# Performance work log

Hardware: AMD Instinct MI355X
Metric: run time of the kernel (lower is better)

## Reference

```python
import jax, jax.numpy as jnp
import numpy as np

MODEL_DIM = 2048
HEAD_DIM = 64
STATE_DIM = 128
EXPAND = 2
CHUNK = 64
INNER = EXPAND * MODEL_DIM          # 4096
NHEADS = INNER // HEAD_DIM          # 64
IN_PROJ = INNER + 2 * STATE_DIM + NHEADS  # 4416
B_SZ = 2
SEQ = 4096


def segsum(x):
    """Stable segment sum: x (..., T) -> (..., T, T) with -inf above diagonal."""
    T = x.shape[-1]
    mask_strict = jnp.tril(jnp.ones((T, T), dtype=bool), -1)
    # element [d, e] = x[d] on strictly-lower triangle, 0 elsewhere
    xt = jnp.where(mask_strict, x[..., :, None], 0.0)
    seg = jnp.cumsum(xt, axis=-2)
    mask = jnp.tril(jnp.ones((T, T), dtype=bool), 0)
    return jnp.where(mask, seg, -jnp.inf)


def ssd(x, A, B, C, chunk):
    """Mamba-2 SSD. x:(b,L,h,p), A:(b,L,h), B/C:(b,L,n) shared over heads."""
    b, L, h, p = x.shape
    n = B.shape[-1]
    c = L // chunk
    x = x.reshape(b, c, chunk, h, p)
    A = A.reshape(b, c, chunk, h).transpose(0, 3, 1, 2)  # (b,h,c,l)
    B = B.reshape(b, c, chunk, n)
    C = C.reshape(b, c, chunk, n)

    A_cs = jnp.cumsum(A, axis=-1)                        # (b,h,c,l)
    Lm = jnp.exp(segsum(A))                              # (b,h,c,l,l)
    # 1. diagonal (intra-chunk) output
    Y_diag = jnp.einsum('bcln,bcsn,bhcls,bcshp->bclhp', C, B, Lm, x)
    # 2. per-chunk states
    decay_states = jnp.exp(A_cs[..., -1:] - A_cs)        # (b,h,c,l)
    states = jnp.einsum('bcln,bhcl,bclhp->bchpn', B, decay_states, x)
    states = jnp.concatenate([jnp.zeros_like(states[:, :1]), states], axis=1)
    # 3. inter-chunk recurrence
    A_chunk = jnp.pad(A_cs[..., -1], ((0, 0), (0, 0), (1, 0)))   # (b,h,c+1)
    decay_chunk = jnp.exp(segsum(A_chunk))               # (b,h,c+1,c+1)
    new_states = jnp.einsum('bhzc,bchpn->bzhpn', decay_chunk, states)
    states_prev, final_state = new_states[:, :-1], new_states[:, -1]
    # 4. state -> output
    Y_off = jnp.einsum('bcln,bchpn,bhcl->bclhp', C, states_prev, jnp.exp(A_cs))
    Y = (Y_diag + Y_off).reshape(b, L, h, p)
    return Y, final_state


def setup_inputs() -> dict:
    key = jax.random.key(0)
    ks = jax.random.split(key, 6)
    u = jax.random.normal(ks[0], (B_SZ, SEQ, MODEL_DIM), jnp.float32)
    W_in = jax.random.normal(ks[1], (IN_PROJ, MODEL_DIM), jnp.float32) * 0.02
    b_in = jnp.zeros((IN_PROJ,), jnp.float32)
    W_out = jax.random.normal(ks[2], (MODEL_DIM, INNER), jnp.float32) * 0.02
    b_out = jnp.zeros((MODEL_DIM,), jnp.float32)
    # A_log = log(uniform(1, 16)) per Mamba-2 init
    A_log = jnp.log(jax.random.uniform(ks[3], (NHEADS,), jnp.float32, 1.0, 16.0))
    # dt_bias = inv-softplus of dt ~ loguniform(1e-3, 1e-1)
    dt = jnp.exp(jax.random.uniform(ks[4], (NHEADS,), jnp.float32)
                 * (np.log(0.1) - np.log(0.001)) + np.log(0.001))
    dt = jnp.clip(dt, 1e-4, None)
    dt_bias = dt + jnp.log(-jnp.expm1(-dt))
    return {'u': u, 'W_in': W_in, 'b_in': b_in, 'W_out': W_out,
            'b_out': b_out, 'A_log': A_log, 'dt_bias': dt_bias}


def reference(u, W_in, b_in, W_out, b_out, A_log, dt_bias):
    xBCdt = u @ W_in.T + b_in                       # (b, L, IN_PROJ)
    x, Bm, Cm, dt = jnp.split(
        xBCdt, [INNER, INNER + STATE_DIM, INNER + 2 * STATE_DIM], axis=-1)
    A = -jnp.exp(A_log)                             # (h,)
    dt = jax.nn.softplus(dt + dt_bias)              # (b, L, h)
    x = x.reshape(B_SZ, SEQ, NHEADS, HEAD_DIM)
    y, final_state = ssd(x * dt[..., None], A * dt, Bm, Cm, CHUNK)
    y = y.reshape(B_SZ, SEQ, INNER)
    y = y @ W_out.T + b_out
    return y, final_state
```

## Files before the change

### kernel.cpp

```cpp
#include <hip/hip_runtime.h>
#include <hip/hip_bf16.h>

typedef __hip_bfloat16 bf16;
typedef __attribute__((ext_vector_type(8))) short short8;
typedef __attribute__((ext_vector_type(4))) float f32x4;

#define MODEL_DIM 2048
#define INNER     4096
#define NHEADS    64
#define HEAD_DIM  64
#define STATE_DIM 128
#define IN_PROJ   4416
#define NPAD      4608
#define BSZ       2
#define SEQ       4096
#define CHUNKL    64
#define NTOK      (BSZ*SEQ)
#define NCHUNK    (SEQ/CHUNKL)

#define WAITV0() asm volatile("s_waitcnt vmcnt(0)" ::: "memory")
#define BAR()    __builtin_amdgcn_s_barrier()
#define SCHEDB() __builtin_amdgcn_sched_barrier(0)
#define WAITLG(N) do { asm volatile("s_waitcnt lgkmcnt(" #N ")" ::: "memory"); SCHEDB(); } while (0)

#define SWZ(x) ((x) ^ ((((x) >> 7) & 7) << 4))

static __device__ __forceinline__ void gload_lds16(const bf16* g, bf16* l) {
  __builtin_amdgcn_global_load_lds((const __attribute__((address_space(1))) void*)g,
                                   (__attribute__((address_space(3))) void*)l, 16, 0, 0);
}

static __device__ __forceinline__ unsigned lds_u32(const void* p) {
  return (unsigned)(unsigned long long)(const __attribute__((address_space(3))) char*)p;
}

static __device__ __forceinline__ short8 ds_read128(unsigned addr) {
  short8 r;
  asm volatile("ds_read_b128 %0, %1" : "=v"(r) : "v"(addr));
  return r;
}

static __device__ __forceinline__ void stage_unit(const bf16* __restrict__ P, int K,
                                                  int blockRow, int kt,
                                                  char* region, int unit, int t) {
  int o = unit * 8192 + (t << 4);
  int lb = SWZ(o);
  int row = lb >> 7, colb = lb & 127;
  gload_lds16(P + (size_t)(blockRow + row) * K + kt + (colb >> 1), (bf16*)(region + o));
}

#define MFMA_BLK(MLO, MHI, NLO, NHI)                                                    \
  __builtin_amdgcn_s_setprio(1);                                                       \
  _Pragma("unroll") for (int mf = (MLO); mf < (MHI); ++mf)                             \
    _Pragma("unroll") for (int nf = (NLO); nf < (NHI); ++nf)                           \
      _Pragma("unroll") for (int ks = 0; ks < 2; ++ks)                                 \
        acc[mf][nf] = __builtin_amdgcn_mfma_f32_16x16x32_bf16(a[mf][ks], b[nf][ks],    \
                                                              acc[mf][nf], 0, 0, 0);  \
  __builtin_amdgcn_s_setprio(0);

template<int BN>
static __device__ __forceinline__ void gemm_core1(
    const bf16* __restrict__ Ag, const bf16* __restrict__ Bg,
    int K, int NT, int bm, int bn, char* lds, f32x4 (&acc)[8][BN / 64]) {
  constexpr int NR = BN / 64;
  constexpr int BB = 32768 + NR * 8192;
  const int t = threadIdx.x;
  const int lane = t & 63;
  const int wid = t >> 6, wm = wid >> 2, wn = wid & 3;
  const unsigned x16 = (unsigned)(lane & 7) << 4;
  const unsigned kb0 = (unsigned)(lane >> 4) << 4;
  const unsigned ldsB = lds_u32(lds);
  const unsigned aRow0 = (unsigned)(wm * 128 + (lane & 15)) * 128;
  const unsigned bRow0 = (unsigned)(wn * (BN / 4) + (lane & 15)) * 128;

#pragma unroll
  for (int u = 0; u < 4; ++u) stage_unit(Ag, K, bm, 0, lds, u, t);
#pragma unroll
  for (int u = 0; u < NR; ++u) stage_unit(Bg, K, bn, 0, lds + 32768, u, t);
  WAITV0();
  BAR();

  int cur = 0;
  for (int tt = 0; tt < NT; ++tt) {
    char* oth = lds + (cur ^ 1) * BB;
    const unsigned aB = ldsB + (unsigned)(cur * BB);
    const unsigned bB = aB + 32768;
    const bool st = (tt + 1 < NT);

    if (st) {
      const int kt1 = (tt + 1) * 64;
#pragma unroll
      for (int u = 0; u < 4; ++u) stage_unit(Ag, K, bm, kt1, oth, u, t);
#pragma unroll
      for (int u = 0; u < NR; ++u) stage_unit(Bg, K, bn, kt1, oth + 32768, u, t);
    }

    short8 a[8][2], b[NR][2];
#pragma unroll
    for (int mf = 0; mf < 4; ++mf)
#pragma unroll
      for (int ks = 0; ks < 2; ++ks)
        a[mf][ks] = ds_read128(aB + aRow0 + mf * 2048 + (((unsigned)(ks * 64) + kb0) ^ x16));
#pragma unroll
    for (int nf = 0; nf < 2; ++nf)
#pragma unroll
      for (int ks = 0; ks < 2; ++ks)
        b[nf][ks] = ds_read128(bB + bRow0 + nf * 2048 + (((unsigned)(ks * 64) + kb0) ^ x16));
#pragma unroll
    for (int mf = 4; mf < 8; ++mf)
#pragma unroll
      for (int ks = 0; ks < 2; ++ks)
        a[mf][ks] = ds_read128(aB + aRow0 + mf * 2048 + (((unsigned)(ks * 64) + kb0) ^ x16));
#pragma unroll
    for (int nf = 2; nf < NR; ++nf)
#pragma unroll
      for (int ks = 0; ks < 2; ++ks)
        b[nf][ks] = ds_read128(bB + bRow0 + nf * 2048 + (((unsigned)(ks * 64) + kb0) ^ x16));

    if constexpr (NR == 4) WAITLG(12); else WAITLG(10);
    MFMA_BLK(0, 4, 0, 2);
    if constexpr (NR == 4) WAITLG(4);  else WAITLG(2);
    MFMA_BLK(4, 8, 0, 2);
    WAITLG(0);
    MFMA_BLK(0, 8, 2, NR);

    if (st) WAITV0();
    BAR();
    cur ^= 1;
  }
}

__global__ __launch_bounds__(512, 2)
void gemm_in256(const bf16* __restrict__ A, const bf16* __restrict__ Bw,
                const float* __restrict__ bias, bf16* __restrict__ x_bf,
                bf16* __restrict__ B_bf, bf16* __restrict__ C_bf, float* __restrict__ dtraw) {
  __shared__ char lds[2 * (32768 + 3 * 8192)];
  int nwg = gridDim.x, bid = blockIdx.x;
  int cpx = nwg >> 3;
  int sb = (bid & 7) * cpx + (bid >> 3);
  int bx = sb % (NPAD / 192), by = sb / (NPAD / 192);
  int bm = by * 256, bn = bx * 192;
  f32x4 acc[8][3] = {};
  gemm_core1<192>(A, Bw, MODEL_DIM, MODEL_DIM / 64, bm, bn, lds, acc);
  const int lane = threadIdx.x & 63, wid = threadIdx.x >> 6;
  const int wm = wid >> 2, wn = wid & 3;
#pragma unroll
  for (int mf = 0; mf < 8; ++mf)
#pragma unroll
    for (int nf = 0; nf < 3; ++nf)
#pragma unroll
      for (int r = 0; r < 4; ++r) {
        int row = bm + wm * 128 + mf * 16 + (lane >> 4) * 4 + r;
        int col = bn + wn * 48 + nf * 16 + (lane & 15);
        float v = acc[mf][nf][r] + ((col < IN_PROJ) ? bias[col] : 0.f);
        if (col < 4096)       x_bf[(size_t)row * 4096 + col]         = __float2bfloat16(v);
        else if (col < 4224)  B_bf[(size_t)row * 128 + (col - 4096)] = __float2bfloat16(v);
        else if (col < 4352)  C_bf[(size_t)row * 128 + (col - 4224)] = __float2bfloat16(v);
        else if (col < 4416)  dtraw[(size_t)row * 64 + (col - 4352)] = v;
      }
}

__global__ __launch_bounds__(512, 2)
void gemm_out256(const bf16* __restrict__ A, const bf16* __restrict__ Bw,
                 const float* __restrict__ bias, float* __restrict__ C) {
  __shared__ char lds[2 * (32768 + 4 * 8192)];
  int nwg = gridDim.x, bid = blockIdx.x;
  int cpx = nwg >> 3;
  int sb = (bid & 7) * cpx + (bid >> 3);
  int bx = sb % (MODEL_DIM / 256), by = sb / (MODEL_DIM / 256);
  int bm = by * 256, bn = bx * 256;
  f32x4 acc[8][4] = {};
  gemm_core1<256>(A, Bw, INNER, INNER / 64, bm, bn, lds, acc);
  const int lane = threadIdx.x & 63, wid = threadIdx.x >> 6;
  const int wm = wid >> 2, wn = wid & 3;
#pragma unroll
  for (int mf = 0; mf < 8; ++mf)
#pragma unroll
    for (int nf = 0; nf < 4; ++nf)
#pragma unroll
      for (int r = 0; r < 4; ++r) {
        int row = bm + wm * 128 + mf * 16 + (lane >> 4) * 4 + r;
        int col = bn + wn * 64 + nf * 16 + (lane & 15);
        C[(size_t)row * MODEL_DIM + col] = acc[mf][nf][r] + bias[col];
      }
}

__global__ __launch_bounds__(256) void conv_f32_to_bf16(const float* __restrict__ src,
                                                        bf16* __restrict__ dst, int n4) {
  int i = blockIdx.x * 256 + threadIdx.x;
  if (i >= n4) return;
  float4 v = *(const float4*)(src + (size_t)i * 4);
  bf16* d = dst + (size_t)i * 4;
  d[0] = __float2bfloat16(v.x); d[1] = __float2bfloat16(v.y);
  d[2] = __float2bfloat16(v.z); d[3] = __float2bfloat16(v.w);
}

__global__ __launch_bounds__(256) void conv_win_pad(const float* __restrict__ W,
                                                    bf16* __restrict__ dst) {
  int i = blockIdx.x * 256 + threadIdx.x;
  int row = (i * 4) >> 11;
  int col = (i * 4) & 2047;
  bf16* d = dst + (size_t)i * 4;
  if (row < IN_PROJ) {
    float4 v = *(const float4*)(W + (size_t)row * 2048 + col);
    d[0] = __float2bfloat16(v.x); d[1] = __float2bfloat16(v.y);
    d[2] = __float2bfloat16(v.z); d[3] = __float2bfloat16(v.w);
  } else {
    bf16 z = __float2bfloat16(0.f);
    d[0] = z; d[1] = z; d[2] = z; d[3] = z;
  }
}

__global__ __launch_bounds__(256)
void prep_small(const float* __restrict__ dtraw, const float* __restrict__ A_log,
                const float* __restrict__ dt_bias, float* __restrict__ dts,
                float* __restrict__ a_dt) {
  int i = blockIdx.x * 256 + threadIdx.x;
  int h = i & 63;
  float z = dtraw[i] + dt_bias[h];
  float dt = (z > 20.f) ? z : log1pf(expf(z));
  dts[i] = dt;
  a_dt[i] = -expf(A_log[h]) * dt;
}

#define LP 72
__global__ __launch_bounds__(256)
void ssd_fused_kernel(const bf16* __restrict__ x_bf, const bf16* __restrict__ B_bf,
                      const float* __restrict__ dts_g, const float* __restrict__ a_dt,
                      float* __restrict__ acs_g, bf16* __restrict__ states_g,
                      float* __restrict__ out_fs) {
  __shared__ bf16 xT[2][32 * LP];
  __shared__ bf16 BT[2][128 * LP];
  __shared__ float sc_s[64];
  __shared__ float dfac_s[1];
  int blk = blockIdx.x;
  int pg = blk & 1, h = (blk >> 1) & 63, b = blk >> 7;
  int t = threadIdx.x, lane = t & 63, w = t >> 6;
  int lx = t >> 2, sx = t & 3;
  int lB = t >> 2, sB = t & 3;

  f32x4 S4[4] = {};
  short8 rx, rB[4]; float ra = 0.f, rdt = 0.f;
  {
    int tb = b * SEQ;
    rx = *(const short8*)(x_bf + (size_t)(tb + lx) * 4096 + h * 64 + pg * 32 + sx * 8);
#pragma unroll
    for (int k = 0; k < 4; ++k)
      rB[k] = *(const short8*)(B_bf + (size_t)(tb + lB) * 128 + sB * 32 + k * 8);
    if (t < 64) { ra = a_dt[(size_t)(tb + t) * 64 + h]; rdt = dts_g[(size_t)(tb + t) * 64 + h]; }
  }

  for (int c = 0; c < 64; ++c) {
    int cn = (c < 63) ? c + 1 : 63;
    int tbn = b * SEQ + cn * 64;
    short8 rx2 = *(const short8*)(x_bf + (size_t)(tbn + lx) * 4096 + h * 64 + pg * 32 + sx * 8);
    short8 rB2[4];
#pragma unroll
    for (int k = 0; k < 4; ++k)
      rB2[k] = *(const short8*)(B_bf + (size_t)(tbn + lB) * 128 + sB * 32 + k * 8);
    float ra2 = 0.f, rdt2 = 0.f;
    if (t < 64) { ra2 = a_dt[(size_t)(tbn + t) * 64 + h]; rdt2 = dts_g[(size_t)(tbn + t) * 64 + h]; }

    if (t < 64) {
      float v = ra;
#pragma unroll
      for (int d = 1; d < 64; d <<= 1) { float o = __shfl_up(v, d); if (t >= d) v += o; }
      float a63 = __shfl(v, 63);
      if (pg == 0) acs_g[(((size_t)(b * 64 + c)) * 64 + h) * 64 + t] = v;
      sc_s[t] = rdt * expf(a63 - v);
      if (t == 0) dfac_s[0] = expf(a63);
    }
    __syncthreads();

    int bufc = c & 1;
    float dfac = dfac_s[0];
    {
      float s_l = sc_s[lx];
      const bf16* pv = (const bf16*)&rx;
#pragma unroll
      for (int j = 0; j < 8; ++j)
        xT[bufc][(sx * 8 + j) * LP + lx] = __float2bfloat16(__bfloat162float(pv[j]) * s_l);
#pragma unroll
      for (int k = 0; k < 4; ++k) {
        const bf16* pb = (const bf16*)&rB[k];
        int n0 = sB * 32 + k * 8;
#pragma unroll
        for (int j = 0; j < 8; ++j) BT[bufc][(n0 + j) * LP + lB] = pb[j];
      }
    }
    __syncthreads();

    int ps = (w >> 1) * 16, nb = (w & 1) * 64;
    f32x4 acc[4] = {};
    short8 af[2];
#pragma unroll
    for (int ks = 0; ks < 2; ++ks)
      af[ks] = *(const short8*)(&xT[bufc][(ps + (lane & 15)) * LP + ks * 32 + (lane >> 4) * 8]);
#pragma unroll
    for (int nf = 0; nf < 4; ++nf)
#pragma unroll
      for (int ks = 0; ks < 2; ++ks) {
        short8 bf_ = *(const short8*)(&BT[bufc][(nb + nf * 16 + (lane & 15)) * LP + ks * 32 + (lane >> 4) * 8]);
        acc[nf] = __builtin_amdgcn_mfma_f32_16x16x32_bf16(af[ks], bf_, acc[nf], 0, 0, 0);
      }
    size_t sbase = ((size_t)((b * 64 + c) * 64 + h)) * 8192;
#pragma unroll
    for (int nf = 0; nf < 4; ++nf)
#pragma unroll
      for (int r = 0; r < 4; ++r) {
        int p = pg * 32 + ps + (lane >> 4) * 4 + r;
        int n = nb + nf * 16 + (lane & 15);
        states_g[sbase + (size_t)p * 128 + n] = __float2bfloat16(S4[nf][r]);
        S4[nf][r] = dfac * S4[nf][r] + acc[nf][r];
      }

    rx = rx2; ra = ra2; rdt = rdt2;
#pragma unroll
    for (int k = 0; k < 4; ++k) rB[k] = rB2[k];
  }

  size_t ob = ((size_t)(b * 64 + h)) * 8192;
  int ps = (w >> 1) * 16, nb = (w & 1) * 64;
#pragma unroll
  for (int nf = 0; nf < 4; ++nf)
#pragma unroll
    for (int r = 0; r < 4; ++r) {
      int p = pg * 32 + ps + (lane >> 4) * 4 + r;
      int n = nb + nf * 16 + (lane & 15);
      out_fs[ob + (size_t)p * 128 + n] = S4[nf][r];
    }
}

__global__ __launch_bounds__(256)
void ssd_out_kernel(bf16* __restrict__ x_bf, const bf16* __restrict__ B_bf,
                    const bf16* __restrict__ C_bf, const float* __restrict__ dts,
                    const float* __restrict__ acs_g, const bf16* __restrict__ states_g) {
  __shared__ bf16 Cs[64 * 128];
  __shared__ bf16 BsMs[64 * 128];
  __shared__ bf16 xT[64 * 64];
  __shared__ bf16 Sp[64 * 128];
  __shared__ float acs_s[64];
  int blk = blockIdx.x;
  int h = blk & 63, c = (blk >> 6) & 63, b = blk >> 12;
  int t = threadIdx.x, lane = t & 63, wid = t >> 6;
  int tokBase = b * SEQ + c * 64;
  size_t sbase = ((size_t)((b * 64 + c) * 64 + h)) * 8192;

  if (t < 64) acs_s[t] = acs_g[(((size_t)(b * 64 + c)) * 64 + h) * 64 + t];
#pragma unroll
  for (int i = 0; i < 4; ++i) {
    int chunk = t + i * 256;
    int l = chunk >> 4, n0 = (chunk & 15) * 8;
    *(short8*)(Cs + l * 128 + n0) = *(const short8*)(C_bf + (size_t)(tokBase + l) * 128 + n0);
    *(short8*)(BsMs + l * 128 + n0) = *(const short8*)(B_bf + (size_t)(tokBase + l) * 128 + n0);
  }
#pragma unroll
  for (int i = 0; i < 2; ++i) {
    int chunk = t + i * 256;
    int l = chunk >> 3, p0 = (chunk & 7) * 8;
    float dtv = dts[(size_t)(tokBase + l) * 64 + h];
    short8 vv = *(const short8*)(x_bf + (size_t)(tokBase + l) * 4096 + h * 64 + p0);
    const bf16* pv = (const bf16*)&vv;
#pragma unroll
    for (int j = 0; j < 8; ++j)
      xT[(p0 + j) * 64 + l] = __float2bfloat16(__bfloat162float(pv[j]) * dtv);
  }
#pragma unroll
  for (int i = 0; i < 4; ++i) {
    int chunk = t + i * 256;
    *(short8*)(Sp + chunk * 8) = *(const short8*)(states_g + sbase + chunk * 8);
  }
  __syncthreads();

  int lBase = (wid >> 1) * 32, sBase = (wid & 1) * 32;
  f32x4 g[2][2] = {};
#pragma unroll
  for (int ks = 0; ks < 4; ++ks) {
    short8 a[2], bb[2];
#pragma unroll
    for (int mi = 0; mi < 2; ++mi)
      a[mi] = *(const short8*)(Cs + (lBase + mi * 16 + (lane & 15)) * 128 + ks * 32 + (lane >> 4) * 8);
#pragma unroll
    for (int ni = 0; ni < 2; ++ni)
      bb[ni] = *(const short8*)(BsMs + (sBase + ni * 16 + (lane & 15)) * 128 + ks * 32 + (lane >> 4) * 8);
#pragma unroll
    for (int mi = 0; mi < 2; ++mi)
#pragma unroll
      for (int ni = 0; ni < 2; ++ni)
        g[mi][ni] = __builtin_amdgcn_mfma_f32_16x16x32_bf16(a[mi], bb[ni], g[mi][ni], 0, 0, 0);
  }
  __syncthreads();

  bf16* Ms = BsMs;
#pragma unroll
  for (int mi = 0; mi < 2; ++mi)
#pragma unroll
    for (int ni = 0; ni < 2; ++ni)
#pragma unroll
      for (int r = 0; r < 4; ++r) {
        int row = lBase + mi * 16 + (lane >> 4) * 4 + r;
        int col = sBase + ni * 16 + (lane & 15);
        float lm = (row >= col) ? expf(acs_s[row] - acs_s[col]) : 0.f;
        Ms[row * 64 + col] = __float2bfloat16(g[mi][ni][r] * lm);
      }
  __syncthreads();

  int pBase = (wid & 1) * 32;
  f32x4 yd[2][2] = {}, yo[2][2] = {};
#pragma unroll
  for (int ks = 0; ks < 2; ++ks) {
    short8 a[2], bb[2];
#pragma unroll
    for (int mi = 0; mi < 2; ++mi)
      a[mi] = *(const short8*)(Ms + (lBase + mi * 16 + (lane & 15)) * 64 + ks * 32 + (lane >> 4) * 8);
#pragma unroll
    for (int ni = 0; ni < 2; ++ni)
      bb[ni] = *(const short8*)(xT + (pBase + ni * 16 + (lane & 15)) * 64 + ks * 32 + (lane >> 4) * 8);
#pragma unroll
    for (int mi = 0; mi < 2; ++mi)
#pragma unroll
      for (int ni = 0; ni < 2; ++ni)
        yd[mi][ni] = __builtin_amdgcn_mfma_f32_16x16x32_bf16(a[mi], bb[ni], yd[mi][ni], 0, 0, 0);
  }
#pragma unroll
  for (int ks = 0; ks < 4; ++ks) {
    short8 a[2], bb[2];
#pragma unroll
    for (int mi = 0; mi < 2; ++mi)
      a[mi] = *(const short8*)(Cs + (lBase + mi * 16 + (lane & 15)) * 128 + ks * 32 + (lane >> 4) * 8);
#pragma unroll
    for (int ni = 0; ni < 2; ++ni)
      bb[ni] = *(const short8*)(Sp + (pBase + ni * 16 + (lane & 15)) * 128 + ks * 32 + (lane >> 4) * 8);
#pragma unroll
    for (int mi = 0; mi < 2; ++mi)
#pragma unroll
      for (int ni = 0; ni < 2; ++ni)
        yo[mi][ni] = __builtin_amdgcn_mfma_f32_16x16x32_bf16(a[mi], bb[ni], yo[mi][ni], 0, 0, 0);
  }
  __syncthreads();
#pragma unroll
  for (int mi = 0; mi < 2; ++mi)
#pragma unroll
    for (int ni = 0; ni < 2; ++ni)
#pragma unroll
      for (int r = 0; r < 4; ++r) {
        int lr = lBase + mi * 16 + (lane >> 4) * 4 + r;
        int p = pBase + ni * 16 + (lane & 15);
        float val = yd[mi][ni][r] + expf(acs_s[lr]) * yo[mi][ni][r];
        x_bf[(size_t)(tokBase + lr) * 4096 + h * 64 + p] = __float2bfloat16(val);
      }
}

extern "C" void kernel_launch(void* const* d_in, const int* in_sizes, int n_in,
                              void* d_out, int out_size, void* d_ws, size_t ws_size,
                              hipStream_t stream) {
  const float* u       = (const float*)d_in[0];
  const float* W_in    = (const float*)d_in[1];
  const float* b_in    = (const float*)d_in[2];
  const float* W_out   = (const float*)d_in[3];
  const float* b_out   = (const float*)d_in[4];
  const float* A_log   = (const float*)d_in[5];
  const float* dt_bias = (const float*)d_in[6];

  float* y_out  = (float*)d_out;
  float* fs_out = y_out + (size_t)NTOK * MODEL_DIM;

  char* ws = (char*)d_ws;
  size_t off = 0;
  auto alloc = [&](size_t bytes) { char* p = ws + off; off += (bytes + 255) & ~255ull; return p; };
  bf16*  wout_bf = (bf16*) alloc((size_t)MODEL_DIM * INNER * 2);
  bf16*  x_bf    = (bf16*) alloc((size_t)NTOK * INNER * 2);
  bf16*  B_bf    = (bf16*) alloc((size_t)NTOK * STATE_DIM * 2);
  bf16*  C_bf    = (bf16*) alloc((size_t)NTOK * STATE_DIM * 2);
  float* dtraw   = (float*)alloc((size_t)NTOK * NHEADS * 4);
  float* dts     = (float*)alloc((size_t)NTOK * NHEADS * 4);
  float* a_dt    = (float*)alloc((size_t)NTOK * NHEADS * 4);
  float* acs     = (float*)alloc((size_t)BSZ * NCHUNK * NHEADS * 64 * 4);
  char*  Q       = alloc((size_t)BSZ * NCHUNK * NHEADS * 64 * 128 * 2);
  bf16*  states  = (bf16*)Q;
  bf16*  u_bf    = (bf16*)Q;
  bf16*  win_bf  = u_bf + (size_t)NTOK * MODEL_DIM;
  (void)ws_size; (void)off; (void)in_sizes; (void)n_in; (void)out_size;

  conv_f32_to_bf16<<<dim3(16384), dim3(256), 0, stream>>>(u, u_bf, NTOK * MODEL_DIM / 4);
  conv_win_pad<<<dim3(NPAD * MODEL_DIM / 1024), dim3(256), 0, stream>>>(W_in, win_bf);
  conv_f32_to_bf16<<<dim3(8192), dim3(256), 0, stream>>>(W_out, wout_bf, MODEL_DIM * INNER / 4);

  gemm_in256<<<dim3((NTOK / 256) * (NPAD / 192)), dim3(512), 0, stream>>>(
      u_bf, win_bf, b_in, x_bf, B_bf, C_bf, dtraw);

  prep_small<<<dim3(NTOK * NHEADS / 256), dim3(256), 0, stream>>>(dtraw, A_log, dt_bias, dts, a_dt);

  ssd_fused_kernel<<<dim3(BSZ * NHEADS * 2), dim3(256), 0, stream>>>(
      x_bf, B_bf, dts, a_dt, acs, states, fs_out);

  ssd_out_kernel<<<dim3(BSZ * NCHUNK * NHEADS), dim3(256), 0, stream>>>(
      x_bf, B_bf, C_bf, dts, acs, states);

  gemm_out256<<<dim3((MODEL_DIM / 256) * (NTOK / 256)), dim3(512), 0, stream>>>(
      x_bf, wout_bf, b_out, y_out);
}
```

Measured before the change: 573.4 us.

## Precompute head-shared C·Bᵀ per chunk and drop W_in padding

Adds a kernel that computes the C·Bᵀ Gram matrix once per chunk, since B and C are shared across heads. ssd_out then loads it instead of recomputing it in every head block. It also removes padding of W_in to 4608 rows, using 23 column tiles of 192 exactly, so the input GEMM does less wasted work and the padded conversion kernel goes away. In exchange, ssd_out reads an extra fp32 matrix from global memory per block, and there is one more kernel launch.

```diff
diff --git a/kernel.cpp b/kernel.cpp
--- a/kernel.cpp
+++ b/kernel.cpp
@@ -11,7 +11,6 @@
 #define HEAD_DIM  64
 #define STATE_DIM 128
 #define IN_PROJ   4416
-#define NPAD      4608
 #define BSZ       2
 #define SEQ       4096
 #define CHUNKL    64
@@ -138,7 +137,7 @@
   int nwg = gridDim.x, bid = blockIdx.x;
   int cpx = nwg >> 3;
   int sb = (bid & 7) * cpx + (bid >> 3);
-  int bx = sb % (NPAD / 192), by = sb / (NPAD / 192);
+  int bx = sb % (IN_PROJ / 192), by = sb / (IN_PROJ / 192);
   int bm = by * 256, bn = bx * 192;
   f32x4 acc[8][3] = {};
   gemm_core1<192>(A, Bw, MODEL_DIM, MODEL_DIM / 64, bm, bn, lds, acc);
@@ -152,11 +151,11 @@
       for (int r = 0; r < 4; ++r) {
         int row = bm + wm * 128 + mf * 16 + (lane >> 4) * 4 + r;
         int col = bn + wn * 48 + nf * 16 + (lane & 15);
-        float v = acc[mf][nf][r] + ((col < IN_PROJ) ? bias[col] : 0.f);
+        float v = acc[mf][nf][r] + bias[col];
         if (col < 4096)       x_bf[(size_t)row * 4096 + col]         = __float2bfloat16(v);
         else if (col < 4224)  B_bf[(size_t)row * 128 + (col - 4096)] = __float2bfloat16(v);
         else if (col < 4352)  C_bf[(size_t)row * 128 + (col - 4224)] = __float2bfloat16(v);
-        else if (col < 4416)  dtraw[(size_t)row * 64 + (col - 4352)] = v;
+        else                  dtraw[(size_t)row * 64 + (col - 4352)] = v;
       }
 }
 
@@ -195,22 +194,6 @@
   d[2] = __float2bfloat16(v.z); d[3] = __float2bfloat16(v.w);
 }
 
-__global__ __launch_bounds__(256) void conv_win_pad(const float* __restrict__ W,
-                                                    bf16* __restrict__ dst) {
-  int i = blockIdx.x * 256 + threadIdx.x;
-  int row = (i * 4) >> 11;
-  int col = (i * 4) & 2047;
-  bf16* d = dst + (size_t)i * 4;
-  if (row < IN_PROJ) {
-    float4 v = *(const float4*)(W + (size_t)row * 2048 + col);
-    d[0] = __float2bfloat16(v.x); d[1] = __float2bfloat16(v.y);
-    d[2] = __float2bfloat16(v.z); d[3] = __float2bfloat16(v.w);
-  } else {
-    bf16 z = __float2bfloat16(0.f);
-    d[0] = z; d[1] = z; d[2] = z; d[3] = z;
-  }
-}
-
 __global__ __launch_bounds__(256)
 void prep_small(const float* __restrict__ dtraw, const float* __restrict__ A_log,
                 const float* __restrict__ dt_bias, float* __restrict__ dts,
@@ -221,6 +204,54 @@
   float dt = (z > 20.f) ? z : log1pf(expf(z));
   dts[i] = dt;
   a_dt[i] = -expf(A_log[h]) * dt;
+}
+
+__global__ __launch_bounds__(256)
+void g_pre_kernel(const bf16* __restrict__ B_bf, const bf16* __restrict__ C_bf,
+                  float* __restrict__ G_g) {
+  __shared__ bf16 Cs[64 * 128];
+  __shared__ bf16 Bs[64 * 128];
+  int blk = blockIdx.x;
+  int t = threadIdx.x, lane = t & 63, wid = t >> 6;
+  int tokBase = (blk >> 6) * SEQ + (blk & 63) * 64;
+
+#pragma unroll
+  for (int i = 0; i < 4; ++i) {
+    int chunk = t + i * 256;
+    int l = chunk >> 4, n0 = (chunk & 15) * 8;
+    *(short8*)(Cs + l * 128 + n0) = *(const short8*)(C_bf + (size_t)(tokBase + l) * 128 + n0);
+    *(short8*)(Bs + l * 128 + n0) = *(const short8*)(B_bf + (size_t)(tokBase + l) * 128 + n0);
+  }
+  __syncthreads();
+
+  int lBase = (wid >> 1) * 32, sBase = (wid & 1) * 32;
+  f32x4 g[2][2] = {};
+#pragma unroll
+  for (int ks = 0; ks < 4; ++ks) {
+    short8 a[2], bb[2];
+#pragma unroll
+    for (int mi = 0; mi < 2; ++mi)
+      a[mi] = *(const short8*)(Cs + (lBase + mi * 16 + (lane & 15)) * 128 + ks * 32 + (lane >> 4) * 8);
+#pragma unroll
+    for (int ni = 0; ni < 2; ++ni)
+      bb[ni] = *(const short8*)(Bs + (sBase + ni * 16 + (lane & 15)) * 128 + ks * 32 + (lane >> 4) * 8);
+#pragma unroll
+    for (int mi = 0; mi < 2; ++mi)
+#pragma unroll
+      for (int ni = 0; ni < 2; ++ni)
+        g[mi][ni] = __builtin_amdgcn_mfma_f32_16x16x32_bf16(a[mi], bb[ni], g[mi][ni], 0, 0, 0);
+  }
+  float* Gd = G_g + (size_t)blk * 4096;
+#pragma unroll
+  for (int mi = 0; mi < 2; ++mi)
+#pragma unroll
+    for (int ni = 0; ni < 2; ++ni)
+#pragma unroll
+      for (int r = 0; r < 4; ++r) {
+        int row = lBase + mi * 16 + (lane >> 4) * 4 + r;
+        int col = sBase + ni * 16 + (lane & 15);
+        Gd[row * 64 + col] = g[mi][ni][r];
+      }
 }
 
 #define LP 72
@@ -332,11 +363,11 @@
 }
 
 __global__ __launch_bounds__(256)
-void ssd_out_kernel(bf16* __restrict__ x_bf, const bf16* __restrict__ B_bf,
-                    const bf16* __restrict__ C_bf, const float* __restrict__ dts,
-                    const float* __restrict__ acs_g, const bf16* __restrict__ states_g) {
+void ssd_out_kernel(bf16* __restrict__ x_bf, const bf16* __restrict__ C_bf,
+                    const float* __restrict__ dts, const float* __restrict__ acs_g,
+                    const bf16* __restrict__ states_g, const float* __restrict__ G_g) {
   __shared__ bf16 Cs[64 * 128];
-  __shared__ bf16 BsMs[64 * 128];
+  __shared__ bf16 Ms[64 * 64];
   __shared__ bf16 xT[64 * 64];
   __shared__ bf16 Sp[64 * 128];
   __shared__ float acs_s[64];
@@ -346,13 +377,24 @@
   int tokBase = b * SEQ + c * 64;
   size_t sbase = ((size_t)((b * 64 + c) * 64 + h)) * 8192;
 
+  int lBase = (wid >> 1) * 32, sBase = (wid & 1) * 32;
+  const float* Gd = G_g + ((size_t)(b * 64 + c)) * 4096;
+  float gv[2][2][4];
+#pragma unroll
+  for (int mi = 0; mi < 2; ++mi)
+#pragma unroll
+    for (int ni = 0; ni < 2; ++ni)
+#pragma unroll
+      for (int r = 0; r < 4; ++r)
+        gv[mi][ni][r] = Gd[(lBase + mi * 16 + (lane >> 4) * 4 + r) * 64 +
+                           sBase + ni * 16 + (lane & 15)];
+
   if (t < 64) acs_s[t] = acs_g[(((size_t)(b * 64 + c)) * 64 + h) * 64 + t];
 #pragma unroll
   for (int i = 0; i < 4; ++i) {
     int chunk = t + i * 256;
     int l = chunk >> 4, n0 = (chunk & 15) * 8;
     *(short8*)(Cs + l * 128 + n0) = *(const short8*)(C_bf + (size_t)(tokBase + l) * 128 + n0);
-    *(short8*)(BsMs + l * 128 + n0) = *(const short8*)(B_bf + (size_t)(tokBase + l) * 128 + n0);
   }
 #pragma unroll
   for (int i = 0; i < 2; ++i) {
@@ -372,26 +414,6 @@
   }
   __syncthreads();
 
-  int lBase = (wid >> 1) * 32, sBase = (wid & 1) * 32;
-  f32x4 g[2][2] = {};
-#pragma unroll
-  for (int ks = 0; ks < 4; ++ks) {
-    short8 a[2], bb[2];
-#pragma unroll
-    for (int mi = 0; mi < 2; ++mi)
-      a[mi] = *(const short8*)(Cs + (lBase + mi * 16 + (lane & 15)) * 128 + ks * 32 + (lane >> 4) * 8);
-#pragma unroll
-    for (int ni = 0; ni < 2; ++ni)
-      bb[ni] = *(const short8*)(BsMs + (sBase + ni * 16 + (lane & 15)) * 128 + ks * 32 + (lane >> 4) * 8);
-#pragma unroll
-    for (int mi = 0; mi < 2; ++mi)
-#pragma unroll
-      for (int ni = 0; ni < 2; ++ni)
-        g[mi][ni] = __builtin_amdgcn_mfma_f32_16x16x32_bf16(a[mi], bb[ni], g[mi][ni], 0, 0, 0);
-  }
-  __syncthreads();
-
-  bf16* Ms = BsMs;
 #pragma unroll
   for (int mi = 0; mi < 2; ++mi)
 #pragma unroll
@@ -401,7 +423,7 @@
         int row = lBase + mi * 16 + (lane >> 4) * 4 + r;
         int col = sBase + ni * 16 + (lane & 15);
         float lm = (row >= col) ? expf(acs_s[row] - acs_s[col]) : 0.f;
-        Ms[row * 64 + col] = __float2bfloat16(g[mi][ni][r] * lm);
+        Ms[row * 64 + col] = __float2bfloat16(gv[mi][ni][r] * lm);
       }
   __syncthreads();
 
@@ -476,6 +498,7 @@
   float* dts     = (float*)alloc((size_t)NTOK * NHEADS * 4);
   float* a_dt    = (float*)alloc((size_t)NTOK * NHEADS * 4);
   float* acs     = (float*)alloc((size_t)BSZ * NCHUNK * NHEADS * 64 * 4);
+  float* gbuf    = (float*)alloc((size_t)BSZ * NCHUNK * 4096 * 4);
   char*  Q       = alloc((size_t)BSZ * NCHUNK * NHEADS * 64 * 128 * 2);
   bf16*  states  = (bf16*)Q;
   bf16*  u_bf    = (bf16*)Q;
@@ -483,19 +506,22 @@
   (void)ws_size; (void)off; (void)in_sizes; (void)n_in; (void)out_size;
 
   conv_f32_to_bf16<<<dim3(16384), dim3(256), 0, stream>>>(u, u_bf, NTOK * MODEL_DIM / 4);
-  conv_win_pad<<<dim3(NPAD * MODEL_DIM / 1024), dim3(256), 0, stream>>>(W_in, win_bf);
+  conv_f32_to_bf16<<<dim3(IN_PROJ * MODEL_DIM / 1024), dim3(256), 0, stream>>>(
+      W_in, win_bf, IN_PROJ * MODEL_DIM / 4);
   conv_f32_to_bf16<<<dim3(8192), dim3(256), 0, stream>>>(W_out, wout_bf, MODEL_DIM * INNER / 4);
 
-  gemm_in256<<<dim3((NTOK / 256) * (NPAD / 192)), dim3(512), 0, stream>>>(
+  gemm_in256<<<dim3((NTOK / 256) * (IN_PROJ / 192)), dim3(512), 0, stream>>>(
       u_bf, win_bf, b_in, x_bf, B_bf, C_bf, dtraw);
 
   prep_small<<<dim3(NTOK * NHEADS / 256), dim3(256), 0, stream>>>(dtraw, A_log, dt_bias, dts, a_dt);
+
+  g_pre_kernel<<<dim3(BSZ * NCHUNK), dim3(256), 0, stream>>>(B_bf, C_bf, gbuf);
 
   ssd_fused_kernel<<<dim3(BSZ * NHEADS * 2), dim3(256), 0, stream>>>(
       x_bf, B_bf, dts, a_dt, acs, states, fs_out);
 
   ssd_out_kernel<<<dim3(BSZ * NCHUNK * NHEADS), dim3(256), 0, stream>>>(
-      x_bf, B_bf, C_bf, dts, acs, states);
+      x_bf, C_bf, dts, acs, states, gbuf);
 
   gemm_out256<<<dim3((MODEL_DIM / 256) * (NTOK / 256)), dim3(512), 0, stream>>>(
       x_bf, wout_bf, b_out, y_out);
```

Result: faster. 509.4 us (-11.2%).
